# Kernel optimization log

Hardware: AMD Instinct MI355X
Metric: run time of the kernel (lower is better)

## Reference

```python
import jax, jax.numpy as jnp
import numpy as np

B, S, D, H = 4, 2048, 1024, 16
HD = D // H


def setup_inputs() -> dict:
    key = jax.random.key(0)
    ks = jax.random.split(key, 5)
    s_in = 1.0 / np.sqrt(D)
    return {
        "x": jax.random.normal(ks[0], (B, S, D), dtype=jnp.float32),
        "W_attn": jax.random.uniform(ks[1], (D, 3 * D), dtype=jnp.float32, minval=-s_in, maxval=s_in),
        "b_attn": jax.random.uniform(ks[2], (3 * D,), dtype=jnp.float32, minval=-s_in, maxval=s_in),
        "W_proj": jax.random.uniform(ks[3], (D, D), dtype=jnp.float32, minval=-s_in, maxval=s_in),
        "b_proj": jax.random.uniform(ks[4], (D,), dtype=jnp.float32, minval=-s_in, maxval=s_in),
    }


def reference(x, W_attn, b_attn, W_proj, b_proj):
    b, s, d = x.shape
    qkv = x @ W_attn + b_attn                      # [B,S,3D]
    q, k, v = jnp.split(qkv, 3, axis=-1)
    # [B,H,S,HD]
    q = q.reshape(b, s, H, HD).transpose(0, 2, 1, 3)
    k = k.reshape(b, s, H, HD).transpose(0, 2, 1, 3)
    v = v.reshape(b, s, H, HD).transpose(0, 2, 1, 3)
    scale = 1.0 / np.sqrt(HD)
    att = jnp.einsum("bhqd,bhkd->bhqk", q, k) * scale
    causal = jnp.tril(jnp.ones((s, s), dtype=bool))
    att = jnp.where(causal[None, None], att, -jnp.inf)
    att = jax.nn.softmax(att, axis=-1)
    y = jnp.einsum("bhqk,bhkd->bhqd", att, v)      # [B,H,S,HD]
    y = y.transpose(0, 2, 1, 3).reshape(b, s, d)
    return y @ W_proj + b_proj
```

## Files before the change

kernel.cpp:

```cpp
#include <hip/hip_runtime.h>

#define B_  4
#define S_  2048
#define D_  1024
#define H_  16
#define HD_ 64
#define BS_ (B_*S_)

typedef _Float16 f16;
typedef _Float16 f16_8 __attribute__((ext_vector_type(8)));
typedef _Float16 f16_4 __attribute__((ext_vector_type(4)));
typedef float    f32_4 __attribute__((ext_vector_type(4)));
typedef unsigned int u32;

#define MFMA32(a,b,c) __builtin_amdgcn_mfma_f32_16x16x32_f16(a, b, c, 0, 0, 0)
#define MFMA16(a,b,c) __builtin_amdgcn_mfma_f32_16x16x16f16(a, b, c, 0, 0, 0)
#define NEG_INF (-__builtin_inff())

__device__ inline void gl_lds16(const f16* g, f16* lds_base, int chunk_base) {
    __builtin_amdgcn_global_load_lds(
        (const __attribute__((address_space(1))) u32*)g,
        (__attribute__((address_space(3))) u32*)(lds_base + (size_t)chunk_base * 8),
        16, 0, 0);
}

__global__ __launch_bounds__(256) void prep(
    const float* __restrict__ X,  f16* __restrict__ Xh,
    const float* __restrict__ Wa, f16* __restrict__ Wta)
{
    __shared__ f16 T[64][72];
    const int t = threadIdx.x;
    const int bid = blockIdx.x;
    if (bid < 4096) {
        const size_t i = ((size_t)bid * 256 + t) * 8;
        float4 a = *(const float4*)&X[i];
        float4 b = *(const float4*)&X[i + 4];
        f16 h[8] = {(f16)a.x,(f16)a.y,(f16)a.z,(f16)a.w,
                    (f16)b.x,(f16)b.y,(f16)b.z,(f16)b.w};
        *(uint4*)&Xh[i] = *(const uint4*)h;
        return;
    }
    const int idx = bid - 4096;
    const int n0 = (idx % 48) * 64, k0 = (idx / 48) * 64;
    const int nl4 = (t & 15) * 4;
    #pragma unroll
    for (int r = 0; r < 4; r++) {
        const int kl = (t >> 4) + r * 16;
        float4 v = *(const float4*)&Wa[(size_t)(k0 + kl) * 3072 + n0 + nl4];
        T[nl4 + 0][kl] = (f16)v.x;
        T[nl4 + 1][kl] = (f16)v.y;
        T[nl4 + 2][kl] = (f16)v.z;
        T[nl4 + 3][kl] = (f16)v.w;
    }
    __syncthreads();
    const int nr = t >> 2, kc = (t & 3) * 16;
    *(uint4*)&Wta[(size_t)(n0 + nr) * 1024 + k0 + kc]     = *(uint4*)&T[nr][kc];
    *(uint4*)&Wta[(size_t)(n0 + nr) * 1024 + k0 + kc + 8] = *(uint4*)&T[nr][kc + 8];
}

__global__ __launch_bounds__(256) void trans_w(
    const float* __restrict__ W, f16* __restrict__ Wt, int ncols)
{
    __shared__ f16 T[64][72];
    const int t = threadIdx.x;
    const int n0 = blockIdx.x * 64, k0 = blockIdx.y * 64;
    const int nl4 = (t & 15) * 4;
    #pragma unroll
    for (int r = 0; r < 4; r++) {
        const int kl = (t >> 4) + r * 16;
        float4 v = *(const float4*)&W[(size_t)(k0 + kl) * ncols + n0 + nl4];
        T[nl4 + 0][kl] = (f16)v.x;
        T[nl4 + 1][kl] = (f16)v.y;
        T[nl4 + 2][kl] = (f16)v.z;
        T[nl4 + 3][kl] = (f16)v.w;
    }
    __syncthreads();
    const int nr = t >> 2, kc = (t & 3) * 16;
    *(uint4*)&Wt[(size_t)(n0 + nr) * 1024 + k0 + kc]     = *(uint4*)&T[nr][kc];
    *(uint4*)&Wt[(size_t)(n0 + nr) * 1024 + k0 + kc + 8] = *(uint4*)&T[nr][kc + 8];
}

__global__ __launch_bounds__(512, 2) void qkv_gemm(
    const f16*   __restrict__ Xh,
    const f16*   __restrict__ Wta,
    const float* __restrict__ bias,
    f16* __restrict__ Qb, f16* __restrict__ Kb, f16* __restrict__ Vt)
{
    __shared__ f16 lds[73728];

    const int t    = threadIdx.x;
    const int lane = t & 63;
    const int w    = t >> 6;
    const int quad = lane >> 4, l15 = lane & 15;
    const int wr = w >> 2, wc = w & 3;
    const int m0 = blockIdx.x * 128;
    const int n0 = blockIdx.y * 256;
    const int wb = t & 448;

    int aoff[2], boff[4];
    #pragma unroll
    for (int c = 0; c < 2; c++) {
        const int i = c*512 + t, row = i >> 3, sl = i & 7;
        aoff[c] = row*1024 + ((sl ^ (row & 7)) << 3);
    }
    #pragma unroll
    for (int c = 0; c < 4; c++) {
        const int i = c*512 + t, row = i >> 3, sl = i & 7;
        boff[c] = row*1024 + ((sl ^ (row & 7)) << 3);
    }
    int fa[4][2], fb[4][2];
    #pragma unroll
    for (int mi = 0; mi < 4; mi++)
        #pragma unroll
        for (int kk = 0; kk < 2; kk++)
            fa[mi][kk] = (wr*64 + mi*16 + l15)*64 + (((kk*4 + quad) ^ (l15 & 7)) << 3);
    #pragma unroll
    for (int ni = 0; ni < 4; ni++)
        #pragma unroll
        for (int kk = 0; kk < 2; kk++)
            fb[ni][kk] = (wc*64 + ni*16 + l15)*64 + (((kk*4 + quad) ^ (l15 & 7)) << 3);

    const f16* Ag = Xh  + (size_t)m0 * 1024;
    const f16* Bg = Wta + (size_t)n0 * 1024;

    f32_4 acc[4][4] = {};

    #pragma unroll
    for (int c = 0; c < 2; c++) gl_lds16(Ag + aoff[c],       lds,                c*512 + wb);
    #pragma unroll
    for (int c = 0; c < 4; c++) gl_lds16(Bg + boff[c],       lds + 8192,         c*512 + wb);
    #pragma unroll
    for (int c = 0; c < 2; c++) gl_lds16(Ag + 64 + aoff[c],  lds + 24576,        c*512 + wb);
    #pragma unroll
    for (int c = 0; c < 4; c++) gl_lds16(Bg + 64 + boff[c],  lds + 24576 + 8192, c*512 + wb);
    asm volatile("s_waitcnt vmcnt(6)" ::: "memory");
    __builtin_amdgcn_s_barrier();
    asm volatile("" ::: "memory");

    int cur = 0;
    #pragma unroll 1
    for (int T = 0; T < 16; T++) {
        f16* buf        = lds + cur*24576;
        const int nxt   = cur ? cur - 1 : 2;
        f16* nbuf       = lds + nxt*24576;
        const bool st   = (T < 14);
        const int  kt2  = (T + 2) * 64;

        if (st) {
            #pragma unroll
            for (int c = 0; c < 2; c++)
                gl_lds16(Ag + kt2 + aoff[c], nbuf, c*512 + wb);
        }
        f16_8 af[4][2], bf[2][2];
        #pragma unroll
        for (int mi = 0; mi < 4; mi++)
            #pragma unroll
            for (int kk = 0; kk < 2; kk++)
                af[mi][kk] = *(const f16_8*)&buf[fa[mi][kk]];
        #pragma unroll
        for (int ni = 0; ni < 2; ni++)
            #pragma unroll
            for (int kk = 0; kk < 2; kk++)
                bf[ni][kk] = *(const f16_8*)&buf[8192 + fb[ni][kk]];
        asm volatile("" ::: "memory");
        __builtin_amdgcn_s_barrier();
        asm volatile("" ::: "memory");
        __builtin_amdgcn_s_setprio(1);
        #pragma unroll
        for (int kk = 0; kk < 2; kk++)
            #pragma unroll
            for (int mi = 0; mi < 4; mi++)
                #pragma unroll
                for (int ni = 0; ni < 2; ni++)
                    acc[mi][ni] = MFMA32(af[mi][kk], bf[ni][kk], acc[mi][ni]);
        __builtin_amdgcn_s_setprio(0);
        asm volatile("" ::: "memory");
        __builtin_amdgcn_s_barrier();
        asm volatile("" ::: "memory");

        if (st) {
            #pragma unroll
            for (int c = 0; c < 4; c++)
                gl_lds16(Bg + kt2 + boff[c], nbuf + 8192, c*512 + wb);
        }
        #pragma unroll
        for (int ni = 0; ni < 2; ni++)
            #pragma unroll
            for (int kk = 0; kk < 2; kk++)
                bf[ni][kk] = *(const f16_8*)&buf[8192 + fb[2 + ni][kk]];
        asm volatile("" ::: "memory");
        __builtin_amdgcn_s_barrier();
        asm volatile("" ::: "memory");
        __builtin_amdgcn_s_setprio(1);
        #pragma unroll
        for (int kk = 0; kk < 2; kk++)
            #pragma unroll
            for (int mi = 0; mi < 4; mi++)
                #pragma unroll
                for (int ni = 0; ni < 2; ni++)
                    acc[mi][2 + ni] = MFMA32(af[mi][kk], bf[ni][kk], acc[mi][2 + ni]);
        __builtin_amdgcn_s_setprio(0);
        if (T < 14)       asm volatile("s_waitcnt vmcnt(6)" ::: "memory");
        else if (T == 14) asm volatile("s_waitcnt vmcnt(0)" ::: "memory");
        __builtin_amdgcn_s_barrier();
        asm volatile("" ::: "memory");

        cur = (cur >= 2) ? 0 : cur + 1;
    }

    const int which = n0 >> 10;
    float bcol[4];
    #pragma unroll
    for (int ni = 0; ni < 4; ni++)
        bcol[ni] = bias[n0 + wc*64 + ni*16 + l15];

    if (which < 2) {
        f16* dst = (which == 0) ? Qb : Kb;
        const float sc = (which == 0) ? 0.125f * 1.44269504f : 1.0f;
        #pragma unroll
        for (int mi = 0; mi < 4; mi++)
        #pragma unroll
        for (int ni = 0; ni < 4; ni++)
        #pragma unroll
        for (int r = 0; r < 4; r++) {
            int m = m0 + wr*64 + mi*16 + quad*4 + r;
            int n = (n0 & 1023) + wc*64 + ni*16 + l15;
            int h = n >> 6, hd = n & 63;
            int b = m >> 11, s = m & 2047;
            dst[((size_t)(b*16 + h)*2048 + s)*64 + hd] =
                (f16)((acc[mi][ni][r] + bcol[ni]) * sc);
        }
    } else {
        f16* Ct = lds;
        #pragma unroll
        for (int mi = 0; mi < 4; mi++)
        #pragma unroll
        for (int ni = 0; ni < 4; ni++)
        #pragma unroll
        for (int r = 0; r < 4; r++) {
            int nl = wc*64 + ni*16 + l15;
            int ml = wr*64 + mi*16 + quad*4 + r;
            Ct[nl*136 + ml] = (f16)(acc[mi][ni][r] + bcol[ni]);
        }
        __syncthreads();
        const int row = t >> 1, half = t & 1;
        const int nv = (n0 & 1023) + row;
        const int h = nv >> 6, hd = nv & 63;
        const int b = m0 >> 11;
        const int s0 = (m0 & 2047) + half*64;
        f16* dst = Vt + ((size_t)(b*16 + h)*64 + hd)*2048 + s0;
        #pragma unroll
        for (int j = 0; j < 8; j++)
            *(uint4*)&dst[j*8] = *(uint4*)&Ct[row*136 + half*64 + j*8];
    }
}

__global__ __launch_bounds__(512, 4) void attn(
    const f16* __restrict__ Qb,
    const f16* __restrict__ Kb,
    const f16* __restrict__ Vt,
    f16* __restrict__ Y)
{
    __shared__ f16 lds[16384];

    const int t    = threadIdx.x;
    const int w    = t >> 6;
    const int lane = t & 63;
    const int quad = lane >> 4, l15 = lane & 15;
    const int bh   = blockIdx.x;
    const int b    = bh >> 4, h = bh & 15;
    const int qbp  = blockIdx.y;
    const int strip = (w < 4) ? qbp : 15 - qbp;
    const int qw   = strip*128 + (w & 3)*32;
    const int NT   = 32 - 2*qbp;

    const f16* qh = Qb + (size_t)bh * S_ * 64;
    const f16* kh = Kb + (size_t)bh * S_ * 64;
    const f16* vt = Vt + (size_t)bh * 64 * S_;

    const int srow = t >> 3;
    const int sgk  = ((t & 7) ^ (srow & 7)) << 3;
    const int wb   = t & 448;
    const int l7   = l15 & 7;
    const f16_4 ones = {(f16)1,(f16)1,(f16)1,(f16)1};

    f16_8 qa[2][2];
    #pragma unroll
    for (int rt = 0; rt < 2; rt++)
        #pragma unroll
        for (int c = 0; c < 2; c++)
            qa[rt][c] = *(const f16_8*)&qh[(size_t)(qw + rt*16 + l15)*64 + c*32 + quad*8];

    f32_4 o[2][4] = {};
    f32_4 lacc[2] = {};

    gl_lds16(kh + (size_t)srow*64 + sgk,  lds,        wb);
    gl_lds16(vt + (size_t)srow*2048 + sgk, lds + 4096, wb);

    #pragma unroll 1
    for (int kt = 0; kt < NT; kt++) {
        const int kbase = kt * 64;
        f16* Ks = lds + (kt & 1) * 8192;
        f16* Vs = Ks + 4096;

        if (kt + 1 < NT) {
            const int nb = kbase + 64;
            f16* nK = lds + ((kt + 1) & 1) * 8192;
            gl_lds16(kh + (size_t)(nb + srow)*64 + sgk, nK,        wb);
            gl_lds16(vt + (size_t)srow*2048 + nb + sgk, nK + 4096, wb);
            asm volatile("s_waitcnt vmcnt(2)" ::: "memory");
        } else {
            asm volatile("s_waitcnt vmcnt(0)" ::: "memory");
        }
        __builtin_amdgcn_s_barrier();
        asm volatile("" ::: "memory");

        if (kbase <= qw + 31) {
            f16_8 kb[4][2];
            #pragma unroll
            for (int sub = 0; sub < 4; sub++)
                #pragma unroll
                for (int c = 0; c < 2; c++)
                    kb[sub][c] = *(const f16_8*)
                        &Ks[(sub*16 + l15)*64 + (((c*4 + quad) ^ l7) << 3)];
            f32_4 st[2][4];
            __builtin_amdgcn_s_setprio(1);
            #pragma unroll
            for (int rt = 0; rt < 2; rt++)
                #pragma unroll
                for (int sub = 0; sub < 4; sub++) {
                    f32_4 a = {};
                    a = MFMA32(kb[sub][0], qa[rt][0], a);
                    a = MFMA32(kb[sub][1], qa[rt][1], a);
                    st[rt][sub] = a;
                }
            __builtin_amdgcn_s_setprio(0);

            const bool masked = (kbase + 63 > qw);
            f16_4 pt[2][4];
            #pragma unroll
            for (int rt = 0; rt < 2; rt++)
            #pragma unroll
            for (int sub = 0; sub < 4; sub++) {
                const int qrow = qw + rt*16 + l15;
                f16_4 p;
                #pragma unroll
                for (int r = 0; r < 4; r++) {
                    float x = st[rt][sub][r];
                    if (masked) {
                        int key = kbase + sub*16 + quad*4 + r;
                        x = (key <= qrow) ? x : NEG_INF;
                    }
                    p[r] = (f16)__builtin_amdgcn_exp2f(x);
                }
                pt[rt][sub] = p;
            }

            #pragma unroll
            for (int rt = 0; rt < 2; rt++) {
                f16_4 ps = (pt[rt][0] + pt[rt][1]) + (pt[rt][2] + pt[rt][3]);
                lacc[rt] = MFMA16(ps, ones, lacc[rt]);
            }

            __builtin_amdgcn_s_setprio(1);
            #pragma unroll
            for (int sub = 0; sub < 4; sub++) {
                f16_4 vb[4];
                #pragma unroll
                for (int tt = 0; tt < 4; tt++)
                    vb[tt] = *(const f16_4*)
                        &Vs[(tt*16 + l15)*64 +
                            ((((sub*2 + (quad >> 1)) ^ l7) << 3) + (quad & 1)*4)];
                #pragma unroll
                for (int rt = 0; rt < 2; rt++)
                    #pragma unroll
                    for (int tt = 0; tt < 4; tt++)
                        o[rt][tt] = MFMA16(pt[rt][sub], vb[tt], o[rt][tt]);
            }
            __builtin_amdgcn_s_setprio(0);
        }
        asm volatile("" ::: "memory");
        __builtin_amdgcn_s_barrier();
        asm volatile("" ::: "memory");
    }

    #pragma unroll
    for (int rt = 0; rt < 2; rt++)
    #pragma unroll
    for (int r = 0; r < 4; r++) {
        float inv = 1.0f / lacc[rt][r];
        int srw = qw + rt*16 + quad*4 + r;
        #pragma unroll
        for (int tt = 0; tt < 4; tt++)
            Y[(size_t)(b*S_ + srw)*1024 + h*64 + tt*16 + l15] =
                (f16)(o[rt][tt][r] * inv);
    }
}

__global__ __launch_bounds__(256) void proj_gemm(
    const f16* __restrict__ Yb,
    const f16* __restrict__ Wtp,
    const float* __restrict__ bias,
    float* __restrict__ Out)
{
    __shared__ f16 lds2[16384];
    f16* Af[2] = {lds2,        lds2 + 4096};
    f16* Bf[2] = {lds2 + 8192, lds2 + 12288};

    const int t    = threadIdx.x;
    const int lane = t & 63;
    const int w    = t >> 6;
    const int quad = lane >> 4, l15 = lane & 15;
    const int wr = w >> 1, wc = w & 1;
    const int m0 = blockIdx.x * 128;
    const int n0 = blockIdx.y * 128;
    const int wbase = t & 192;

    f32_4 acc[4][4] = {};

    for (int k0 = 0; k0 < 1024; k0 += 64) {
        #pragma unroll
        for (int kc = 0; kc < 2; kc++)
            #pragma unroll
            for (int c = 0; c < 2; c++) {
                int i = c*256 + t;
                const int row = i >> 2, col = (i & 3) * 8;
                gl_lds16(Yb  + (size_t)(m0 + row)*1024 + k0 + kc*32 + col,
                         Af[kc], c*256 + wbase);
                gl_lds16(Wtp + (size_t)(n0 + row)*1024 + k0 + kc*32 + col,
                         Bf[kc], c*256 + wbase);
            }
        __syncthreads();
        #pragma unroll
        for (int kc = 0; kc < 2; kc++) {
            f16_8 af[4], bf[4];
            #pragma unroll
            for (int mi = 0; mi < 4; mi++)
                af[mi] = *(const f16_8*)&Af[kc][(wr*64 + mi*16 + l15)*32 + quad*8];
            #pragma unroll
            for (int ni = 0; ni < 4; ni++)
                bf[ni] = *(const f16_8*)&Bf[kc][(wc*64 + ni*16 + l15)*32 + quad*8];
            #pragma unroll
            for (int mi = 0; mi < 4; mi++)
                #pragma unroll
                for (int ni = 0; ni < 4; ni++)
                    acc[mi][ni] = MFMA32(af[mi], bf[ni], acc[mi][ni]);
        }
        __syncthreads();
    }

    #pragma unroll
    for (int mi = 0; mi < 4; mi++)
    #pragma unroll
    for (int ni = 0; ni < 4; ni++)
    #pragma unroll
    for (int r = 0; r < 4; r++) {
        int m = m0 + wr*64 + mi*16 + quad*4 + r;
        int n = n0 + wc*64 + ni*16 + l15;
        Out[(size_t)m*1024 + n] = acc[mi][ni][r] + bias[n];
    }
}

extern "C" void kernel_launch(void* const* d_in, const int* in_sizes, int n_in,
                              void* d_out, int out_size, void* d_ws, size_t ws_size,
                              hipStream_t stream) {
    const float* x      = (const float*)d_in[0];
    const float* W_attn = (const float*)d_in[1];
    const float* b_attn = (const float*)d_in[2];
    const float* W_proj = (const float*)d_in[3];
    const float* b_proj = (const float*)d_in[4];
    float* out = (float*)d_out;

    const size_t per = (size_t)B_ * H_ * S_ * HD_;
    f16* Yb  = (f16*)d_ws;
    f16* Wta = Yb;
    f16* Qb  = Yb + per;
    f16* Kb  = Qb + per;
    f16* Vt  = Kb + per;
    f16* Wtp = Qb;
    f16* Xh  = (f16*)d_out;

    prep     <<<4096 + 768, 256, 0, stream>>>(x, Xh, W_attn, Wta);
    qkv_gemm <<<dim3(64, 12), 512, 0, stream>>>(Xh, Wta, b_attn, Qb, Kb, Vt);
    attn     <<<dim3(64, 8),  512, 0, stream>>>(Qb, Kb, Vt, Yb);
    trans_w  <<<dim3(16, 16), 256, 0, stream>>>(W_proj, Wtp, D_);
    proj_gemm<<<dim3(64, 8),  256, 0, stream>>>(Yb, Wtp, b_proj, out);
}
```

Measured before the change: 263.7 us.

## Split attention blocks into one query strip per 256-thread block, longest first

The attention kernel previously paired a short and a long causal query strip in one 512-thread block to balance work. Now each 256-thread block handles a single 128-row strip, with blockIdx.y mapped so the longest strips launch first, and the grid doubles to 64x16. Each thread now issues two LDS-direct loads per tile instead of one, since fewer threads share the same K/V tile. This trades the paired-strip load balance for smaller, more schedulable blocks, but K/V tiles are no longer shared between the two strips, which raises global traffic.

```diff
diff --git a/kernel.cpp b/kernel.cpp
--- a/kernel.cpp
+++ b/kernel.cpp
@@ -255,7 +255,7 @@
     }
 }
 
-__global__ __launch_bounds__(512, 4) void attn(
+__global__ __launch_bounds__(256, 4) void attn(
     const f16* __restrict__ Qb,
     const f16* __restrict__ Kb,
     const f16* __restrict__ Vt,
@@ -269,19 +269,24 @@
     const int quad = lane >> 4, l15 = lane & 15;
     const int bh   = blockIdx.x;
     const int b    = bh >> 4, h = bh & 15;
-    const int qbp  = blockIdx.y;
-    const int strip = (w < 4) ? qbp : 15 - qbp;
-    const int qw   = strip*128 + (w & 3)*32;
-    const int NT   = 32 - 2*qbp;
+    const int strip = 15 - (int)blockIdx.y;
+    const int qw   = strip*128 + w*32;
+    const int NT   = 2*strip + 2;
 
     const f16* qh = Qb + (size_t)bh * S_ * 64;
     const f16* kh = Kb + (size_t)bh * S_ * 64;
     const f16* vt = Vt + (size_t)bh * 64 * S_;
 
-    const int srow = t >> 3;
-    const int sgk  = ((t & 7) ^ (srow & 7)) << 3;
-    const int wb   = t & 448;
-    const int l7   = l15 & 7;
+    int srcK[2], srcV[2];
+    #pragma unroll
+    for (int c = 0; c < 2; c++) {
+        const int i = c*256 + t, row = i >> 3, sl = i & 7;
+        const int sw = ((sl ^ (row & 7)) << 3);
+        srcK[c] = row*64   + sw;
+        srcV[c] = row*2048 + sw;
+    }
+    const int wbase = t & 192;
+    const int l7    = l15 & 7;
     const f16_4 ones = {(f16)1,(f16)1,(f16)1,(f16)1};
 
     f16_8 qa[2][2];
@@ -294,8 +299,11 @@
     f32_4 o[2][4] = {};
     f32_4 lacc[2] = {};
 
-    gl_lds16(kh + (size_t)srow*64 + sgk,  lds,        wb);
-    gl_lds16(vt + (size_t)srow*2048 + sgk, lds + 4096, wb);
+    #pragma unroll
+    for (int c = 0; c < 2; c++) {
+        gl_lds16(kh + srcK[c], lds,        c*256 + wbase);
+        gl_lds16(vt + srcV[c], lds + 4096, c*256 + wbase);
+    }
 
     #pragma unroll 1
     for (int kt = 0; kt < NT; kt++) {
@@ -306,9 +314,12 @@
         if (kt + 1 < NT) {
             const int nb = kbase + 64;
             f16* nK = lds + ((kt + 1) & 1) * 8192;
-            gl_lds16(kh + (size_t)(nb + srow)*64 + sgk, nK,        wb);
-            gl_lds16(vt + (size_t)srow*2048 + nb + sgk, nK + 4096, wb);
-            asm volatile("s_waitcnt vmcnt(2)" ::: "memory");
+            #pragma unroll
+            for (int c = 0; c < 2; c++) {
+                gl_lds16(kh + (size_t)nb*64 + srcK[c], nK,        c*256 + wbase);
+                gl_lds16(vt + nb + srcV[c],            nK + 4096, c*256 + wbase);
+            }
+            asm volatile("s_waitcnt vmcnt(4)" ::: "memory");
         } else {
             asm volatile("s_waitcnt vmcnt(0)" ::: "memory");
         }
@@ -482,7 +493,7 @@
 
     prep     <<<4096 + 768, 256, 0, stream>>>(x, Xh, W_attn, Wta);
     qkv_gemm <<<dim3(64, 12), 512, 0, stream>>>(Xh, Wta, b_attn, Qb, Kb, Vt);
-    attn     <<<dim3(64, 8),  512, 0, stream>>>(Qb, Kb, Vt, Yb);
+    attn     <<<dim3(64, 16), 256, 0, stream>>>(Qb, Kb, Vt, Yb);
     trans_w  <<<dim3(16, 16), 256, 0, stream>>>(W_proj, Wtp, D_);
     proj_gemm<<<dim3(64, 8),  256, 0, stream>>>(Yb, Wtp, b_proj, out);
 }
```

Result: no change. 266.9 us (+1.2%).
